# Kernel tuning notes

Measured on AMD Instinct MI355X. Metric: run time of the kernel, lower is better.

The kernel has to match this reference:

```python
import jax, jax.numpy as jnp
import numpy as np

N = 50000
E = 800000
IN_DIM = 64
HID = 64
OUT = 40


def setup_inputs() -> dict:
    key = jax.random.key(0)
    ks = jax.random.split(key, 10)
    x = jax.random.normal(ks[0], (N, IN_DIM), dtype=jnp.float32)
    edge_index = jax.random.randint(ks[1], (2, E), 0, N, dtype=jnp.int64)

    def lin(k, fan_in, fan_out):
        # torch nn.Linear default init: U(-1/sqrt(fan_in), 1/sqrt(fan_in))
        bound = 1.0 / np.sqrt(fan_in)
        kw, kb = jax.random.split(k)
        W = jax.random.uniform(kw, (fan_in, fan_out), minval=-bound, maxval=bound, dtype=jnp.float32)
        b = jax.random.uniform(kb, (fan_out,), minval=-bound, maxval=bound, dtype=jnp.float32)
        return W, b

    W1, b1 = lin(ks[2], IN_DIM, HID)   # conv layer 1
    W2, b2 = lin(ks[3], HID, HID)      # conv layer 2
    Wp1, bp1 = lin(ks[4], HID, HID)    # post_mp linear 1
    Wp2, bp2 = lin(ks[5], HID, OUT)    # post_mp linear 2
    return {"x": x, "edge_index": edge_index,
            "W1": W1, "b1": b1, "W2": W2, "b2": b2,
            "Wp1": Wp1, "bp1": bp1, "Wp2": Wp2, "bp2": bp2}


def _mean_aggregate(h, src, dst, num_nodes):
    # Row-normalized sparse adjacency matmul: out[i] = (1/deg(i)) * sum_{(i,j) in E} h[j]
    # adj[src, dst] = 1/deg(src), where deg(src) = #outgoing edges of src.
    ones = jnp.ones((src.shape[0],), dtype=h.dtype)
    deg = jax.ops.segment_sum(ones, src, num_segments=num_nodes)
    w = 1.0 / deg[src]                         # [E], every src has deg >= 1
    msgs = h[dst] * w[:, None]                 # [E, d] gather + scale
    return jax.ops.segment_sum(msgs, src, num_segments=num_nodes)  # [N, d]


def reference(x, edge_index, W1, b1, W2, b2, Wp1, bp1, Wp2, bp2):
    src = edge_index[0]
    dst = edge_index[1]
    n = x.shape[0]
    # GraphSAGEConvolution layer 1: (dropout=eval noop) linear -> spmm mean-agg -> relu
    h = x @ W1 + b1
    h = _mean_aggregate(h, src, dst, n)
    h = jax.nn.relu(h)
    # GraphSAGEConvolution layer 2
    h = h @ W2 + b2
    h = _mean_aggregate(h, src, dst, n)
    h = jax.nn.relu(h)
    # post_mp: Linear -> (dropout noop) -> Linear
    h = h @ Wp1 + bp1
    h = h @ Wp2 + bp2
    return jax.nn.log_softmax(h, axis=1)
```

## Files before the change

kernel.cpp:

```cpp
#include <hip/hip_runtime.h>
#include <cmath>


typedef _Float16 half_t;
typedef half_t half2_t __attribute__((ext_vector_type(2)));
typedef half_t half4_t __attribute__((ext_vector_type(4)));
typedef half_t half8_t __attribute__((ext_vector_type(8)));

#if defined(__has_builtin)
# if __has_builtin(__builtin_amdgcn_fdot2)
#  define FDOT2(a, b, c) __builtin_amdgcn_fdot2((a), (b), (c), false)
# endif
#endif
#ifndef FDOT2
# define FDOT2(a, b, c) fmaf((float)(a)[0], (float)(b)[0], fmaf((float)(a)[1], (float)(b)[1], (c)))
#endif

#define NXCD 8
#define CAP  64
#define EDGE_BLOCKS 2048

__global__ __launch_bounds__(256) void build_h1(
    const int* __restrict__ src, const int* __restrict__ dst,
    const float* __restrict__ x, const float* __restrict__ W1,
    const float* __restrict__ b1,
    const float* __restrict__ W2, const float* __restrict__ Wp1,
    const float* __restrict__ Wp2,
    half_t* __restrict__ Wt, int* __restrict__ cnt,
    unsigned short* __restrict__ col, half_t* __restrict__ Hh,
    int E, int N)
{
    const int tid = threadIdx.x;

    if (blockIdx.x < EDGE_BLOCKS) {
        int gid = blockIdx.x * 256 + tid;
        if (gid < 3 * 4096) {
            int which = gid >> 12, r = gid & 4095;
            int i = r >> 9, c = (r >> 3) & 63, j = r & 7;
            int k = i * 8 + j;
            float v;
            if      (which == 0) v = W2[k * 64 + c];
            else if (which == 1) v = Wp1[k * 64 + c];
            else                 v = (c < 40) ? Wp2[k * 40 + c] : 0.f;
            Wt[gid] = (half_t)v;
        }

        const int g     = blockIdx.x & (NXCD - 1);
        const int bpg   = blockIdx.x >> 3;
        const int nbpg  = EDGE_BLOCKS >> 3;
        const int chunk = (N + NXCD - 1) / NXCD;
        const int lo = g * chunk;
        const int hi = min(N, lo + chunk);
        const int4* src4 = (const int4*)src;
        const int4* dst4 = (const int4*)dst;
        const int quads = E >> 2;
        for (int q = bpg * 256 + tid; q < quads; q += nbpg * 256) {
            int4 s4 = src4[q];
            bool any = (s4.x >= lo && s4.x < hi) || (s4.y >= lo && s4.y < hi) ||
                       (s4.z >= lo && s4.z < hi) || (s4.w >= lo && s4.w < hi);
            if (!any) continue;
            int4 d4 = dst4[q];
            if (s4.x >= lo && s4.x < hi) {
                int pos = atomicAdd(&cnt[s4.x], 1);
                if (pos < CAP) col[(size_t)s4.x * CAP + pos] = (unsigned short)d4.x;
            }
            if (s4.y >= lo && s4.y < hi) {
                int pos = atomicAdd(&cnt[s4.y], 1);
                if (pos < CAP) col[(size_t)s4.y * CAP + pos] = (unsigned short)d4.y;
            }
            if (s4.z >= lo && s4.z < hi) {
                int pos = atomicAdd(&cnt[s4.z], 1);
                if (pos < CAP) col[(size_t)s4.z * CAP + pos] = (unsigned short)d4.z;
            }
            if (s4.w >= lo && s4.w < hi) {
                int pos = atomicAdd(&cnt[s4.w], 1);
                if (pos < CAP) col[(size_t)s4.w * CAP + pos] = (unsigned short)d4.w;
            }
        }
        if (blockIdx.x == 0 && tid < (E & 3)) {
            int e = (E & ~3) + tid;
            int s = src[e];
            int pos = atomicAdd(&cnt[s], 1);
            if (pos < CAP) col[(size_t)s * CAP + pos] = (unsigned short)dst[e];
        }
    } else {
        __shared__ half_t xs[16][64];
        const int lane = tid & 63;
        const int wid  = tid >> 6;
        const int row0 = (blockIdx.x - EDGE_BLOCKS) * 16;

        for (int i = tid; i < 16 * 64; i += 256) {
            int rr = row0 + (i >> 6);
            float v = (rr < N) ? x[(size_t)row0 * 64 + i] : 0.f;
            xs[i >> 6][i & 63] = (half_t)v;
        }
        const float bias = b1[lane];
        __syncthreads();

        float acc[4] = {bias, bias, bias, bias};
#pragma unroll 1
        for (int c = 0; c < 4; ++c) {
            half2_t wr[8];
#pragma unroll
            for (int j = 0; j < 8; ++j) {
                float a0 = W1[(c * 16 + 2 * j + 0) * 64 + lane];
                float a1 = W1[(c * 16 + 2 * j + 1) * 64 + lane];
                half2_t h; h[0] = (half_t)a0; h[1] = (half_t)a1;
                wr[j] = h;
            }
#pragma unroll
            for (int r = 0; r < 4; ++r) {
                const half2_t* xp = (const half2_t*)&xs[wid * 4 + r][c * 16];
#pragma unroll
                for (int j = 0; j < 8; ++j) acc[r] = FDOT2(xp[j], wr[j], acc[r]);
            }
        }
#pragma unroll
        for (int r = 0; r < 4; ++r) {
            int grow = row0 + wid * 4 + r;
            if (grow < N) Hh[(size_t)grow * 64 + lane] = (half_t)acc[r];
        }
    }
}

__device__ __forceinline__ void gather_node(const char* __restrict__ Hbytes,
                                            const unsigned short* __restrict__ cbase,
                                            int deg, int grp, int suboff, float* f) {
    const int myo = ((int)cbase[threadIdx.x & 63]) << 7;
    f[0] = f[1] = f[2] = f[3] = 0.f;
    const int full = deg & ~15;
    int e = 0;
    for (; e < full; e += 16) {
        half4_t hacc; hacc[0] = (half_t)0.f; hacc[1] = (half_t)0.f;
        hacc[2] = (half_t)0.f; hacc[3] = (half_t)0.f;
#pragma unroll
        for (int i = 0; i < 4; ++i) {
            int off = __shfl(myo, e + 4 * i + grp);
            hacc += *(const half4_t*)(Hbytes + off + suboff);
        }
        f[0] += (float)hacc[0]; f[1] += (float)hacc[1];
        f[2] += (float)hacc[2]; f[3] += (float)hacc[3];
    }
    if (e < deg) {
        half4_t hacc; hacc[0] = (half_t)0.f; hacc[1] = (half_t)0.f;
        hacc[2] = (half_t)0.f; hacc[3] = (half_t)0.f;
#pragma unroll
        for (int i = 0; i < 4; ++i) {
            int idx = e + 4 * i + grp;
            int off = __shfl(myo, idx & 63);
            if (idx < deg) hacc += *(const half4_t*)(Hbytes + off + suboff);
        }
        f[0] += (float)hacc[0]; f[1] += (float)hacc[1];
        f[2] += (float)hacc[2]; f[3] += (float)hacc[3];
    }
#pragma unroll
    for (int k = 0; k < 4; ++k) {
        f[k] += __shfl_xor(f[k], 16);
        f[k] += __shfl_xor(f[k], 32);
    }
}

__device__ __forceinline__ void stage_w(const half_t* __restrict__ Wt,
                                        half_t* __restrict__ wlds, int tid, int nthr) {
    const uint4* ws = (const uint4*)Wt;
    uint4* wd = (uint4*)wlds;
    for (int i = tid; i < 512; i += nthr) wd[i] = ws[i];
}

__device__ __forceinline__ void dot64_b128(const half_t* __restrict__ xrow,
                                           const half_t* __restrict__ wlds,
                                           int lane, float& a0, float& a1) {
    const half8_t* wl8 = (const half8_t*)wlds;
    const half8_t* xp8 = (const half8_t*)xrow;
#pragma unroll
    for (int i = 0; i < 8; ++i) {
        half8_t wv = wl8[i * 64 + lane];
        half8_t xv = xp8[i];
        const half2_t* w2 = (const half2_t*)&wv;
        const half2_t* x2 = (const half2_t*)&xv;
        a0 = FDOT2(x2[0], w2[0], a0);
        a1 = FDOT2(x2[1], w2[1], a1);
        a0 = FDOT2(x2[2], w2[2], a0);
        a1 = FDOT2(x2[3], w2[3], a1);
    }
}

__global__ __launch_bounds__(512) void fused_gather_gemm(
    const half_t* __restrict__ H, const int* __restrict__ cnt,
    const unsigned short* __restrict__ colb, const half_t* __restrict__ Wt,
    const float* __restrict__ b, half_t* __restrict__ Y, int N)
{
    __shared__ __align__(16) half_t wlds[4096];
    __shared__ __align__(16) half_t xrow[8][64];
    const int tid  = threadIdx.x;
    const int w    = tid >> 6;
    const int lane = tid & 63;
    const int grp  = lane >> 4;
    const int sub  = lane & 15;

    stage_w(Wt, wlds, tid, 512);
    __syncthreads();

    const int node = blockIdx.x * 8 + w;
    if (node >= N) return;

    const int deg = cnt[node];
    float f[4];
    gather_node((const char*)H, colb + (size_t)node * CAP, deg, grp, sub * 8, f);
    if (grp == 0) {
        float inv = (deg > 0) ? 1.f / (float)deg : 0.f;
        half4_t o;
        o[0] = (half_t)fmaxf(f[0] * inv, 0.f);
        o[1] = (half_t)fmaxf(f[1] * inv, 0.f);
        o[2] = (half_t)fmaxf(f[2] * inv, 0.f);
        o[3] = (half_t)fmaxf(f[3] * inv, 0.f);
        ((half4_t*)xrow[w])[sub] = o;
    }

    float a0 = b[lane], a1 = 0.f;
    dot64_b128(xrow[w], wlds, lane, a0, a1);
    Y[(size_t)node * 64 + lane] = (half_t)(a0 + a1);
}

__global__ __launch_bounds__(256) void gemm40_softmax(const half_t* __restrict__ H3,
                                                      const half_t* __restrict__ Wt2,
                                                      const float* __restrict__ bp2,
                                                      float* __restrict__ out, int n) {
    __shared__ __align__(16) half_t xs[16][64];
    __shared__ __align__(16) half_t wlds[4096];
    const int tid  = threadIdx.x;
    const int lane = tid & 63;
    const int wid  = tid >> 6;
    const int row0 = blockIdx.x * 16;

    stage_w(Wt2, wlds, tid, 256);
    {
        const half2_t* X2 = (const half2_t*)H3;
        half2_t z; z[0] = (half_t)0.f; z[1] = (half_t)0.f;
        for (int i = tid; i < 16 * 32; i += 256) {
            int rr = row0 + (i >> 5);
            ((half2_t*)xs)[i] = (rr < n) ? X2[(size_t)row0 * 32 + i] : z;
        }
    }
    const float bias2 = (lane < 40) ? bp2[lane] : 0.f;
    __syncthreads();

    float a0[4] = {bias2, bias2, bias2, bias2};
    float a1[4] = {0.f, 0.f, 0.f, 0.f};
    const half8_t* wl8 = (const half8_t*)wlds;
#pragma unroll
    for (int i = 0; i < 8; ++i) {
        half8_t wv = wl8[i * 64 + lane];
        const half2_t* w2 = (const half2_t*)&wv;
#pragma unroll
        for (int r = 0; r < 4; ++r) {
            half8_t xv = ((const half8_t*)&xs[wid * 4 + r][0])[i];
            const half2_t* x2 = (const half2_t*)&xv;
            a0[r] = FDOT2(x2[0], w2[0], a0[r]);
            a1[r] = FDOT2(x2[1], w2[1], a1[r]);
            a0[r] = FDOT2(x2[2], w2[2], a0[r]);
            a1[r] = FDOT2(x2[3], w2[3], a1[r]);
        }
    }

#pragma unroll
    for (int r = 0; r < 4; ++r) {
        float acc = a0[r] + a1[r];
        float vm = (lane < 40) ? acc : -INFINITY;
        float m = vm;
#pragma unroll
        for (int o = 32; o; o >>= 1) m = fmaxf(m, __shfl_xor(m, o));
        float e = (lane < 40) ? expf(vm - m) : 0.f;
        float s = e;
#pragma unroll
        for (int o = 32; o; o >>= 1) s += __shfl_xor(s, o);
        float ls = logf(s);
        const int grow = row0 + wid * 4 + r;
        if (grow < n && lane < 40) out[(size_t)grow * 40 + lane] = vm - m - ls;
    }
}

extern "C" void kernel_launch(void* const* d_in, const int* in_sizes, int n_in,
                              void* d_out, int out_size, void* d_ws, size_t ws_size,
                              hipStream_t stream) {
    const float* x   = (const float*)d_in[0];
    const int*   ei  = (const int*)d_in[1];
    const float* W1  = (const float*)d_in[2];
    const float* b1  = (const float*)d_in[3];
    const float* W2  = (const float*)d_in[4];
    const float* b2  = (const float*)d_in[5];
    const float* Wp1 = (const float*)d_in[6];
    const float* bp1 = (const float*)d_in[7];
    const float* Wp2 = (const float*)d_in[8];
    const float* bp2 = (const float*)d_in[9];
    float* out = (float*)d_out;

    const int N = in_sizes[0] / 64;
    const int E = in_sizes[1] / 2;
    const int* src = ei;
    const int* dst = ei + E;

    char*  wsb = (char*)d_ws;
    size_t off = 0;
    auto alloc = [&](size_t bytes) { void* p = wsb + off; off += (bytes + 511) & ~(size_t)511; return p; };
    int*            cnt = (int*)alloc((size_t)N * 4);
    unsigned short* col = (unsigned short*)alloc((size_t)N * CAP * 2);
    half_t*         Wt  = (half_t*)alloc((size_t)3 * 4096 * 2);
    half_t*         Ha  = (half_t*)alloc((size_t)N * 64 * 2);
    half_t*         Hb  = (half_t*)alloc((size_t)N * 64 * 2);
    (void)ws_size; (void)n_in; (void)out_size;

    const int nb16 = (N + 15) / 16;
    const int nb8  = (N + 7) / 8;

    hipMemsetAsync(cnt, 0, (size_t)N * 4, stream);
    build_h1<<<EDGE_BLOCKS + nb16, 256, 0, stream>>>(src, dst, x, W1, b1, W2, Wp1, Wp2,
                                                     Wt, cnt, col, Ha, E, N);
    fused_gather_gemm<<<nb8, 512, 0, stream>>>(Ha, cnt, col, Wt + 0 * 4096, b2, Hb, N);
    fused_gather_gemm<<<nb8, 512, 0, stream>>>(Hb, cnt, col, Wt + 1 * 4096, bp1, Ha, N);
    gemm40_softmax<<<nb16, 256, 0, stream>>>(Ha, Wt + 2 * 4096, bp2, out, N);
}
```

Before: 128.0 us.

## Replace repeated range-filtered edge scans with two-pass bucketed CSR build

Adjacency building used to have each of 8 block groups scan the full edge list and keep only sources in its node range. That read src about eight times. Now a first pass reads each edge once and bins it by source range into one of 8 global buckets. Slots within a block come from shared-memory counters, and each block does one global atomic per bucket. A new second kernel walks each bucket with blocks mapped by blockIdx&7 and fills per-node col lists, which keeps the per-node atomics clustered by range. In exchange it adds a kernel launch and writes and re-reads a packed 32-bit edge buffer, and it assumes node ids fit in 16 bits and each bucket holds at most BC edges.

```diff
diff --git a/kernel.cpp b/kernel.cpp
--- a/kernel.cpp
+++ b/kernel.cpp
@@ -16,23 +16,23 @@
 # define FDOT2(a, b, c) fmaf((float)(a)[0], (float)(b)[0], fmaf((float)(a)[1], (float)(b)[1], (c)))
 #endif
 
-#define NXCD 8
 #define CAP  64
-#define EDGE_BLOCKS 2048
-
-__global__ __launch_bounds__(256) void build_h1(
+#define PA_BLOCKS 784
+#define PB_BLOCKS 2048
+#define BC  131072
+
+__global__ __launch_bounds__(256) void passA_h1(
     const int* __restrict__ src, const int* __restrict__ dst,
     const float* __restrict__ x, const float* __restrict__ W1,
     const float* __restrict__ b1,
     const float* __restrict__ W2, const float* __restrict__ Wp1,
     const float* __restrict__ Wp2,
-    half_t* __restrict__ Wt, int* __restrict__ cnt,
-    unsigned short* __restrict__ col, half_t* __restrict__ Hh,
-    int E, int N)
+    half_t* __restrict__ Wt, unsigned* __restrict__ buf, int* __restrict__ gcur,
+    half_t* __restrict__ Hh, int E, int N, float inv8)
 {
     const int tid = threadIdx.x;
 
-    if (blockIdx.x < EDGE_BLOCKS) {
+    if (blockIdx.x < PA_BLOCKS) {
         int gid = blockIdx.x * 256 + tid;
         if (gid < 3 * 4096) {
             int which = gid >> 12, r = gid & 4095;
@@ -45,49 +45,51 @@
             Wt[gid] = (half_t)v;
         }
 
-        const int g     = blockIdx.x & (NXCD - 1);
-        const int bpg   = blockIdx.x >> 3;
-        const int nbpg  = EDGE_BLOCKS >> 3;
-        const int chunk = (N + NXCD - 1) / NXCD;
-        const int lo = g * chunk;
-        const int hi = min(N, lo + chunk);
-        const int4* src4 = (const int4*)src;
-        const int4* dst4 = (const int4*)dst;
+        __shared__ int lcnt[8];
+        __shared__ int lbase[8];
+        if (tid < 8) lcnt[tid] = 0;
+        __syncthreads();
+
         const int quads = E >> 2;
-        for (int q = bpg * 256 + tid; q < quads; q += nbpg * 256) {
-            int4 s4 = src4[q];
-            bool any = (s4.x >= lo && s4.x < hi) || (s4.y >= lo && s4.y < hi) ||
-                       (s4.z >= lo && s4.z < hi) || (s4.w >= lo && s4.w < hi);
-            if (!any) continue;
-            int4 d4 = dst4[q];
-            if (s4.x >= lo && s4.x < hi) {
-                int pos = atomicAdd(&cnt[s4.x], 1);
-                if (pos < CAP) col[(size_t)s4.x * CAP + pos] = (unsigned short)d4.x;
+        const int q = blockIdx.x * 256 + tid;
+        int ss[4], dd[4], bkt[4], lpos[4];
+        const bool have = q < quads;
+        if (have) {
+            int4 s4 = ((const int4*)src)[q];
+            int4 d4 = ((const int4*)dst)[q];
+            ss[0] = s4.x; ss[1] = s4.y; ss[2] = s4.z; ss[3] = s4.w;
+            dd[0] = d4.x; dd[1] = d4.y; dd[2] = d4.z; dd[3] = d4.w;
+#pragma unroll
+            for (int i = 0; i < 4; ++i) {
+                int b = (int)((float)ss[i] * inv8);
+                bkt[i]  = min(7, max(0, b));
+                lpos[i] = atomicAdd(&lcnt[bkt[i]], 1);
             }
-            if (s4.y >= lo && s4.y < hi) {
-                int pos = atomicAdd(&cnt[s4.y], 1);
-                if (pos < CAP) col[(size_t)s4.y * CAP + pos] = (unsigned short)d4.y;
-            }
-            if (s4.z >= lo && s4.z < hi) {
-                int pos = atomicAdd(&cnt[s4.z], 1);
-                if (pos < CAP) col[(size_t)s4.z * CAP + pos] = (unsigned short)d4.z;
-            }
-            if (s4.w >= lo && s4.w < hi) {
-                int pos = atomicAdd(&cnt[s4.w], 1);
-                if (pos < CAP) col[(size_t)s4.w * CAP + pos] = (unsigned short)d4.w;
+        }
+        __syncthreads();
+        if (tid < 8 && lcnt[tid] > 0) lbase[tid] = atomicAdd(&gcur[tid], lcnt[tid]);
+        __syncthreads();
+        if (have) {
+#pragma unroll
+            for (int i = 0; i < 4; ++i) {
+                int p = lbase[bkt[i]] + lpos[i];
+                if (p < BC)
+                    buf[(size_t)bkt[i] * BC + p] =
+                        (unsigned)ss[i] | ((unsigned)dd[i] << 16);
             }
         }
         if (blockIdx.x == 0 && tid < (E & 3)) {
             int e = (E & ~3) + tid;
-            int s = src[e];
-            int pos = atomicAdd(&cnt[s], 1);
-            if (pos < CAP) col[(size_t)s * CAP + pos] = (unsigned short)dst[e];
+            int s = src[e], d = dst[e];
+            int b = min(7, max(0, (int)((float)s * inv8)));
+            int p = atomicAdd(&gcur[b], 1);
+            if (p < BC) buf[(size_t)b * BC + p] = (unsigned)s | ((unsigned)d << 16);
         }
     } else {
         __shared__ half_t xs[16][64];
         const int lane = tid & 63;
         const int wid  = tid >> 6;
-        const int row0 = (blockIdx.x - EDGE_BLOCKS) * 16;
+        const int row0 = (blockIdx.x - PA_BLOCKS) * 16;
 
         for (int i = tid; i < 16 * 64; i += 256) {
             int rr = row0 + (i >> 6);
@@ -120,6 +122,23 @@
             int grow = row0 + wid * 4 + r;
             if (grow < N) Hh[(size_t)grow * 64 + lane] = (half_t)acc[r];
         }
+    }
+}
+
+__global__ __launch_bounds__(256) void passB(const unsigned* __restrict__ buf,
+                                             const int* __restrict__ gcur,
+                                             int* __restrict__ cnt,
+                                             unsigned short* __restrict__ col) {
+    const int g = blockIdx.x & 7;
+    const int stride = (PB_BLOCKS >> 3) * 256;
+    const int bcount = min(gcur[g], BC);
+    const unsigned* bb = buf + (size_t)g * BC;
+    for (int i = (blockIdx.x >> 3) * 256 + threadIdx.x; i < bcount; i += stride) {
+        unsigned v = bb[i];
+        int s = (int)(v & 0xFFFFu);
+        int d = (int)(v >> 16);
+        int pos = atomicAdd(&cnt[s], 1);
+        if (pos < CAP) col[(size_t)s * CAP + pos] = (unsigned short)d;
     }
 }
 
@@ -303,19 +322,24 @@
     char*  wsb = (char*)d_ws;
     size_t off = 0;
     auto alloc = [&](size_t bytes) { void* p = wsb + off; off += (bytes + 511) & ~(size_t)511; return p; };
-    int*            cnt = (int*)alloc((size_t)N * 4);
-    unsigned short* col = (unsigned short*)alloc((size_t)N * CAP * 2);
-    half_t*         Wt  = (half_t*)alloc((size_t)3 * 4096 * 2);
-    half_t*         Ha  = (half_t*)alloc((size_t)N * 64 * 2);
-    half_t*         Hb  = (half_t*)alloc((size_t)N * 64 * 2);
+    int*            cntz = (int*)alloc((size_t)(N + 8) * 4);
+    unsigned*       buf  = (unsigned*)alloc((size_t)8 * BC * 4);
+    unsigned short* col  = (unsigned short*)alloc((size_t)N * CAP * 2);
+    half_t*         Wt   = (half_t*)alloc((size_t)3 * 4096 * 2);
+    half_t*         Ha   = (half_t*)alloc((size_t)N * 64 * 2);
+    half_t*         Hb   = (half_t*)alloc((size_t)N * 64 * 2);
+    int* cnt  = cntz;
+    int* gcur = cntz + N;
     (void)ws_size; (void)n_in; (void)out_size;
 
     const int nb16 = (N + 15) / 16;
     const int nb8  = (N + 7) / 8;
-
-    hipMemsetAsync(cnt, 0, (size_t)N * 4, stream);
-    build_h1<<<EDGE_BLOCKS + nb16, 256, 0, stream>>>(src, dst, x, W1, b1, W2, Wp1, Wp2,
-                                                     Wt, cnt, col, Ha, E, N);
+    const float inv8 = 8.0f / (float)N;
+
+    hipMemsetAsync(cntz, 0, (size_t)(N + 8) * 4, stream);
+    passA_h1<<<PA_BLOCKS + nb16, 256, 0, stream>>>(src, dst, x, W1, b1, W2, Wp1, Wp2,
+                                                   Wt, buf, gcur, Ha, E, N, inv8);
+    passB<<<PB_BLOCKS, 256, 0, stream>>>(buf, gcur, cnt, col);
     fused_gather_gemm<<<nb8, 512, 0, stream>>>(Ha, cnt, col, Wt + 0 * 4096, b2, Hb, N);
     fused_gather_gemm<<<nb8, 512, 0, stream>>>(Hb, cnt, col, Wt + 1 * 4096, bp1, Ha, N);
     gemm40_softmax<<<nb16, 256, 0, stream>>>(Ha, Wt + 2 * 4096, bp2, out, N);
```

Result: slower. 136.7 us (+6.8%).
